# Performance work log

Hardware: AMD Instinct MI355X
Metric: run time of the kernel (lower is better)

Reference implementation:

```python
import jax, jax.numpy as jnp
import numpy as np

B, T, V, E_DIM, M_DIM, H = 32, 256, 10000, 300, 128, 256


def setup_inputs() -> dict:
    key = jax.random.key(0)
    ks = jax.random.split(key, 8)
    sc = 0.05
    words = jax.random.randint(ks[0], (B, T), 0, V)            # int token ids, 0 = pad
    midis = jax.random.normal(ks[1], (B, T, M_DIM), dtype=jnp.float32)
    E  = jax.random.normal(ks[2], (V, E_DIM), dtype=jnp.float32) * sc   # embedding table
    Wm = jax.random.normal(ks[3], (M_DIM, E_DIM), dtype=jnp.float32) * sc  # midi Dense
    bm = jnp.zeros((E_DIM,), jnp.float32)
    Wx = jax.random.normal(ks[4], (E_DIM, 3 * H), dtype=jnp.float32) * sc  # GRU input kernel [z|r|h]
    bx = jnp.zeros((3 * H,), jnp.float32)
    U  = jax.random.normal(ks[5], (H, 3 * H), dtype=jnp.float32) * sc      # GRU recurrent kernel
    bu = jnp.zeros((3 * H,), jnp.float32)                                  # recurrent bias (reset_after)
    Wo = jax.random.normal(ks[6], (H, V), dtype=jnp.float32) * sc          # output Dense
    bo = jnp.zeros((V,), jnp.float32)
    return {"words": words, "midis": midis, "E": E, "Wm": Wm, "bm": bm,
            "Wx": Wx, "bx": bx, "U": U, "bu": bu, "Wo": Wo, "bo": bo}


def _gru_masked(x, mask, Wx, bx, U, bu):
    """Keras GRU (reset_after=True) with mask carry-through. x: [B,T,E], mask: [B,T] bool."""
    gx = x @ Wx + bx                      # [B,T,3H] precomputed input gates
    gx_t = jnp.swapaxes(gx, 0, 1)         # [T,B,3H]
    m_t = mask.T                          # [T,B]
    h0 = jnp.zeros((x.shape[0], H), x.dtype)

    def step(h, inp):
        g, m = inp
        gh = h @ U + bu                   # [B,3H]
        xz, xr, xn = jnp.split(g, 3, axis=-1)
        hz, hr, hn = jnp.split(gh, 3, axis=-1)
        z = jax.nn.sigmoid(xz + hz)
        r = jax.nn.sigmoid(xr + hr)
        n = jnp.tanh(xn + r * hn)         # reset_after: r applied to recurrent projection
        h_new = z * h + (1.0 - z) * n
        h_new = jnp.where(m[:, None], h_new, h)  # masked step: carry state/output
        return h_new, h_new

    h_last, seq = jax.lax.scan(step, h0, (gx_t, m_t))
    return jnp.swapaxes(seq, 0, 1), h_last  # [B,T,H], [B,H]


def reference(words, midis, E, Wm, bm, Wx, bx, U, bu, Wo, bo):
    mask = words != 0                      # Embedding(mask_zero=True).compute_mask
    x = E[words] + (midis @ Wm + bm)       # [B,T,E] fused embedding + dense add
    seq, _ = _gru_masked(x, mask, Wx, bx, U, bu)
    return seq @ Wo + bo                   # [B,T,V] logits
```

## Files before the change

kernel.cpp:

```cpp
#include <hip/hip_runtime.h>
#include <hip/hip_fp16.h>

typedef unsigned short ushort_t;
typedef short bf16x8 __attribute__((ext_vector_type(8)));
typedef float f32x4 __attribute__((ext_vector_type(4)));
typedef _Float16 f16x8 __attribute__((ext_vector_type(8)));

#define B_SZ 32
#define T_SZ 256
#define V_SZ 10000
#define E_DIM 300
#define M_DIM 128
#define H_SZ 256

__device__ __forceinline__ ushort_t f2bf(float f) {
  unsigned u = __float_as_uint(f);
  unsigned r = u + 0x7fffu + ((u >> 16) & 1u);
  return (ushort_t)(r >> 16);
}

__device__ __forceinline__ void stage16(const void* g, void* l) {
  __builtin_amdgcn_global_load_lds((const __attribute__((address_space(1))) void*)g,
                                   (__attribute__((address_space(3))) void*)l, 16, 0, 0);
}

__global__ void k_cast_bf16(const float* __restrict__ in, ushort_t* __restrict__ out, int n) {
  int i = blockIdx.x * blockDim.x + threadIdx.x;
  if (i < n) out[i] = f2bf(in[i]);
}

template <int MODE>
__global__ void k_transpose_cast(const float* __restrict__ in, ushort_t* __restrict__ out,
                                 int R, int C, int Rp, int Cp) {
  __shared__ float tile[32][33];
  int c0 = blockIdx.x * 32, r0 = blockIdx.y * 32;
  int tx = threadIdx.x, ty = threadIdx.y;
#pragma unroll
  for (int i = 0; i < 32; i += 8) {
    int r = r0 + ty + i, c = c0 + tx;
    tile[ty + i][tx] = (r < R && c < C) ? in[(size_t)r * C + c] : 0.f;
  }
  __syncthreads();
#pragma unroll
  for (int i = 0; i < 32; i += 8) {
    int c = c0 + ty + i, r = r0 + tx;
    if (c < Cp && r < Rp) {
      float v = tile[tx][ty + i];
      if (MODE == 0) {
        out[(size_t)c * Rp + r] = f2bf(v);
      } else {
        __half h = __float2half(v);
        out[(size_t)c * Rp + r] = *(ushort_t*)&h;
      }
    }
  }
}

__global__ void k_xfuse(const float* __restrict__ xtmp, const float* __restrict__ E,
                        const int* __restrict__ words, ushort_t* __restrict__ xb) {
  int m = blockIdx.x;
  int kp = threadIdx.x;
  int w = words[m];
  float v = 0.f;
  if (kp < E_DIM) v = xtmp[(size_t)m * 320 + kp] + E[(size_t)w * E_DIM + kp];
  xb[(size_t)m * 320 + kp] = f2bf(v);
}

__global__ __launch_bounds__(256, 2) void k_gemm_bt(
    const ushort_t* __restrict__ A, const ushort_t* __restrict__ BT,
    const float* __restrict__ bias, float* __restrict__ C,
    int M, int K, int Nreal, int ldc) {
  __shared__ __align__(16) ushort_t As[128 * 64];
  __shared__ __align__(16) ushort_t Bs[128 * 64];
  const int tid = threadIdx.x;
  const int lane = tid & 63;
  const int w = tid >> 6;
  const int wr = w >> 1, wc = w & 1;
  const int m0 = blockIdx.x * 128;
  const int n0 = blockIdx.y * 128;

  f32x4 acc[4][4];
#pragma unroll
  for (int i = 0; i < 4; ++i)
#pragma unroll
    for (int j = 0; j < 4; ++j) acc[i][j] = (f32x4){0.f, 0.f, 0.f, 0.f};

  const int chunk_l = w * 64 + lane;

  for (int k0 = 0; k0 < K; k0 += 64) {
    __syncthreads();
#pragma unroll
    for (int it = 0; it < 4; ++it) {
      const int chunk = it * 256 + chunk_l;
      const int row = chunk >> 3, c = chunk & 7;
      const int base = it * 256 + w * 64;
      stage16(A + (size_t)(m0 + row) * K + k0 + c * 8, (void*)(As + base * 8));
      stage16(BT + (size_t)(n0 + row) * K + k0 + c * 8, (void*)(Bs + base * 8));
    }
    __syncthreads();

    bf16x8 af[4][2], bfr[4][2];
#pragma unroll
    for (int mi = 0; mi < 4; ++mi) {
      int r = wr * 64 + mi * 16 + (lane & 15);
#pragma unroll
      for (int kk = 0; kk < 2; ++kk) {
        int c16 = kk * 4 + (lane >> 4);
        af[mi][kk] = *(const bf16x8*)(As + r * 64 + c16 * 8);
      }
    }
#pragma unroll
    for (int ni = 0; ni < 4; ++ni) {
      int r = wc * 64 + ni * 16 + (lane & 15);
#pragma unroll
      for (int kk = 0; kk < 2; ++kk) {
        int c16 = kk * 4 + (lane >> 4);
        bfr[ni][kk] = *(const bf16x8*)(Bs + r * 64 + c16 * 8);
      }
    }
#pragma unroll
    for (int mi = 0; mi < 4; ++mi)
#pragma unroll
      for (int ni = 0; ni < 4; ++ni)
#pragma unroll
        for (int kk = 0; kk < 2; ++kk)
          acc[mi][ni] = __builtin_amdgcn_mfma_f32_16x16x32_bf16(af[mi][kk], bfr[ni][kk],
                                                                acc[mi][ni], 0, 0, 0);
  }

  const int rbase = m0 + wr * 64 + (lane >> 4) * 4;
  const int cbase = n0 + wc * 64 + (lane & 15);
#pragma unroll
  for (int ni = 0; ni < 4; ++ni) {
    int n = cbase + ni * 16;
    if (n < Nreal) {
      float bn = bias[n];
#pragma unroll
      for (int mi = 0; mi < 4; ++mi) {
#pragma unroll
        for (int rg = 0; rg < 4; ++rg) {
          int mrow = rbase + mi * 16 + rg;
          C[(size_t)mrow * ldc + n] = acc[mi][ni][rg] + bn;
        }
      }
    }
  }
}

__global__ __launch_bounds__(512, 2) void k_gru(
    const float* __restrict__ gx, const ushort_t* __restrict__ UT,
    const float* __restrict__ bu, const int* __restrict__ words,
    ushort_t* __restrict__ seqb) {
  const int b = blockIdx.x;
  const int tid = threadIdx.x;
  const int lane = tid & 63;
  const int w = tid >> 6;

  __shared__ __align__(16) _Float16 hlds[16 * 256];
  __shared__ float ghbuf[768];
  __shared__ int words_s[T_SZ];

  for (int i = tid; i < 16 * 256; i += 512) hlds[i] = (_Float16)0.f;
  if (tid < T_SZ) words_s[tid] = words[b * T_SZ + tid];

  f16x8 Ufrag[6][8];
  {
    const int n0 = w * 96;
    const ushort_t* src = UT + (size_t)(n0 + (lane & 15)) * 256 + (lane >> 4) * 8;
#pragma unroll
    for (int ni = 0; ni < 6; ++ni) {
#pragma unroll
      for (int kk = 0; kk < 8; ++kk)
        Ufrag[ni][kk] = *(const f16x8*)(src + (size_t)ni * 16 * 256 + kk * 32);
    }
  }
  float buz = 0.f, bur = 0.f, bun = 0.f;
  if (tid < H_SZ) {
    buz = bu[tid];
    bur = bu[H_SZ + tid];
    bun = bu[2 * H_SZ + tid];
  }
  __syncthreads();

  const float* gxp = gx + (size_t)b * T_SZ * 768;
  float gxz = 0.f, gxr = 0.f, gxn = 0.f;
  if (tid < H_SZ) {
    gxz = gxp[tid];
    gxr = gxp[H_SZ + tid];
    gxn = gxp[2 * H_SZ + tid];
  }
  float h_old = 0.f;

  const int arow = lane & 15;
  const int abase = arow * 512;
  const int asub = lane >> 4;
  const int aswz = arow & 7;

  for (int t = 0; t < T_SZ; ++t) {
    float gxz_n = 0.f, gxr_n = 0.f, gxn_n = 0.f;
    if (t + 1 < T_SZ && tid < H_SZ) {
      const float* g1 = gxp + (size_t)(t + 1) * 768;
      gxz_n = g1[tid];
      gxr_n = g1[H_SZ + tid];
      gxn_n = g1[2 * H_SZ + tid];
    }

    f32x4 acc[6];
#pragma unroll
    for (int ni = 0; ni < 6; ++ni) acc[ni] = (f32x4){0.f, 0.f, 0.f, 0.f};
#pragma unroll
    for (int kk = 0; kk < 8; ++kk) {
      int c = kk * 4 + asub;
      f16x8 afrag = *(const f16x8*)((const char*)hlds + abase + ((c ^ aswz) << 4));
#pragma unroll
      for (int ni = 0; ni < 6; ++ni)
        acc[ni] = __builtin_amdgcn_mfma_f32_16x16x32_f16(afrag, Ufrag[ni][kk], acc[ni], 0, 0, 0);
    }
    if (lane < 16) {
      const int nb = w * 96 + lane;
#pragma unroll
      for (int ni = 0; ni < 6; ++ni) ghbuf[nb + ni * 16] = acc[ni][0];
    }
    __syncthreads();

    if (tid < H_SZ) {
      float hz = ghbuf[tid] + buz;
      float hr = ghbuf[H_SZ + tid] + bur;
      float hn = ghbuf[2 * H_SZ + tid] + bun;
      float z = 1.f / (1.f + __expf(-(gxz + hz)));
      float r = 1.f / (1.f + __expf(-(gxr + hr)));
      float nv = 2.f / (1.f + __expf(-2.f * (gxn + r * hn))) - 1.f;
      float hnew = (words_s[t] != 0) ? (z * h_old + (1.f - z) * nv) : h_old;
      h_old = hnew;
      seqb[((size_t)b * T_SZ + t) * H_SZ + tid] = f2bf(hnew);
      hlds[tid] = (_Float16)hnew;
    }
    __syncthreads();
    gxz = gxz_n;
    gxr = gxr_n;
    gxn = gxn_n;
  }
}

extern "C" void kernel_launch(void* const* d_in, const int* in_sizes, int n_in,
                              void* d_out, int out_size, void* d_ws, size_t ws_size,
                              hipStream_t stream) {
  const int*   words = (const int*)d_in[0];
  const float* midis = (const float*)d_in[1];
  const float* E     = (const float*)d_in[2];
  const float* Wm    = (const float*)d_in[3];
  const float* bm    = (const float*)d_in[4];
  const float* Wx    = (const float*)d_in[5];
  const float* bx    = (const float*)d_in[6];
  const float* U     = (const float*)d_in[7];
  const float* bu    = (const float*)d_in[8];
  const float* Wo    = (const float*)d_in[9];
  const float* bo    = (const float*)d_in[10];
  float* out = (float*)d_out;

  const int MT = B_SZ * T_SZ;
  size_t off = 0;
  auto alloc = [&](size_t bytes) -> void* {
    void* p = (char*)d_ws + off;
    off += (bytes + 255) & ~(size_t)255;
    return p;
  };
  ushort_t* mid_b = (ushort_t*)alloc((size_t)MT * 128 * 2);
  ushort_t* WmT   = (ushort_t*)alloc((size_t)384 * 128 * 2);
  float*    xtmp  = (float*)   alloc((size_t)MT * 320 * 4);
  ushort_t* x_b   = (ushort_t*)alloc((size_t)MT * 320 * 2);
  ushort_t* WxT   = (ushort_t*)alloc((size_t)768 * 320 * 2);
  float*    gx    = (float*)   alloc((size_t)MT * 768 * 4);
  ushort_t* UT    = (ushort_t*)alloc((size_t)768 * 256 * 2);
  ushort_t* seq_b = (ushort_t*)alloc((size_t)MT * 256 * 2);
  ushort_t* WoT   = (ushort_t*)alloc((size_t)10112 * 256 * 2);
  (void)ws_size;

  k_cast_bf16<<<(MT * 128 + 255) / 256, 256, 0, stream>>>(midis, mid_b, MT * 128);
  k_transpose_cast<0><<<dim3(12, 4),  dim3(32, 8), 0, stream>>>(Wm, WmT, 128, 300, 128, 384);
  k_transpose_cast<0><<<dim3(24, 10), dim3(32, 8), 0, stream>>>(Wx, WxT, 300, 768, 320, 768);
  k_transpose_cast<0><<<dim3(316, 8), dim3(32, 8), 0, stream>>>(Wo, WoT, 256, 10000, 256, 10112);
  k_transpose_cast<1><<<dim3(24, 8),  dim3(32, 8), 0, stream>>>(U, UT, 256, 768, 256, 768);

  k_gemm_bt<<<dim3(64, 3), 256, 0, stream>>>(mid_b, WmT, bm, xtmp, MT, 128, 300, 320);
  k_xfuse<<<MT, 320, 0, stream>>>(xtmp, E, words, x_b);
  k_gemm_bt<<<dim3(64, 6), 256, 0, stream>>>(x_b, WxT, bx, gx, MT, 320, 768, 768);
  k_gru<<<B_SZ, 512, 0, stream>>>(gx, UT, bu, words, seq_b);
  k_gemm_bt<<<dim3(64, 79), 256, 0, stream>>>(seq_b, WoT, bo, out, MT, 256, 10000, 10000);
}
```

Baseline: 471.2 us.

## Remap GRU gate columns per wave and double-buffer hidden state to drop barrier

Each wave now owns matching z/r/n columns for 32 hidden units, so it can do the gate nonlinearities directly from its MFMA accumulators instead of going through a shared gh buffer. The hidden state is double-buffered in LDS, which leaves one __syncthreads per timestep instead of two. The recurrent bias is folded into the accumulator initialisation. In exchange, only 16 lanes per wave do the elementwise work, each handling two units, and gx is loaded with a strided pattern.

```diff
diff --git a/kernel.cpp b/kernel.cpp
--- a/kernel.cpp
+++ b/kernel.cpp
@@ -156,89 +156,94 @@
   const int lane = tid & 63;
   const int w = tid >> 6;
 
-  __shared__ __align__(16) _Float16 hlds[16 * 256];
-  __shared__ float ghbuf[768];
+  __shared__ __align__(16) _Float16 hbuf[2][16 * 256];
   __shared__ int words_s[T_SZ];
 
-  for (int i = tid; i < 16 * 256; i += 512) hlds[i] = (_Float16)0.f;
+  for (int i = tid; i < 2 * 16 * 256; i += 512) hbuf[0][i] = (_Float16)0.f;
   if (tid < T_SZ) words_s[tid] = words[b * T_SZ + tid];
 
+  const int jb = w * 32;
+  int colbase[6] = {jb, jb + 16, H_SZ + jb, H_SZ + jb + 16, 2 * H_SZ + jb, 2 * H_SZ + jb + 16};
+
   f16x8 Ufrag[6][8];
-  {
-    const int n0 = w * 96;
-    const ushort_t* src = UT + (size_t)(n0 + (lane & 15)) * 256 + (lane >> 4) * 8;
-#pragma unroll
-    for (int ni = 0; ni < 6; ++ni) {
-#pragma unroll
-      for (int kk = 0; kk < 8; ++kk)
-        Ufrag[ni][kk] = *(const f16x8*)(src + (size_t)ni * 16 * 256 + kk * 32);
-    }
-  }
-  float buz = 0.f, bur = 0.f, bun = 0.f;
-  if (tid < H_SZ) {
-    buz = bu[tid];
-    bur = bu[H_SZ + tid];
-    bun = bu[2 * H_SZ + tid];
-  }
-  __syncthreads();
-
+#pragma unroll
+  for (int ni = 0; ni < 6; ++ni) {
+    const ushort_t* src = UT + (size_t)(colbase[ni] + (lane & 15)) * 256 + (lane >> 4) * 8;
+#pragma unroll
+    for (int kk = 0; kk < 8; ++kk)
+      Ufrag[ni][kk] = *(const f16x8*)(src + kk * 32);
+  }
+  float bub[6];
+#pragma unroll
+  for (int ni = 0; ni < 6; ++ni) bub[ni] = (lane < 16) ? bu[colbase[ni] + lane] : 0.f;
+
+  const int j0 = jb + (lane & 15);
+  const int j1 = j0 + 16;
   const float* gxp = gx + (size_t)b * T_SZ * 768;
-  float gxz = 0.f, gxr = 0.f, gxn = 0.f;
-  if (tid < H_SZ) {
-    gxz = gxp[tid];
-    gxr = gxp[H_SZ + tid];
-    gxn = gxp[2 * H_SZ + tid];
-  }
-  float h_old = 0.f;
+
+  float gz0 = 0.f, gz1 = 0.f, gr0 = 0.f, gr1 = 0.f, gn0 = 0.f, gn1 = 0.f;
+  if (lane < 16) {
+    gz0 = gxp[j0];          gz1 = gxp[j1];
+    gr0 = gxp[H_SZ + j0];   gr1 = gxp[H_SZ + j1];
+    gn0 = gxp[2 * H_SZ + j0]; gn1 = gxp[2 * H_SZ + j1];
+  }
+  float h0 = 0.f, h1 = 0.f;
 
   const int arow = lane & 15;
   const int abase = arow * 512;
   const int asub = lane >> 4;
   const int aswz = arow & 7;
 
+  int p = 0;
+  __syncthreads();
+
   for (int t = 0; t < T_SZ; ++t) {
-    float gxz_n = 0.f, gxr_n = 0.f, gxn_n = 0.f;
-    if (t + 1 < T_SZ && tid < H_SZ) {
+    float gz0n = 0.f, gz1n = 0.f, gr0n = 0.f, gr1n = 0.f, gn0n = 0.f, gn1n = 0.f;
+    if (t + 1 < T_SZ && lane < 16) {
       const float* g1 = gxp + (size_t)(t + 1) * 768;
-      gxz_n = g1[tid];
-      gxr_n = g1[H_SZ + tid];
-      gxn_n = g1[2 * H_SZ + tid];
+      gz0n = g1[j0];          gz1n = g1[j1];
+      gr0n = g1[H_SZ + j0];   gr1n = g1[H_SZ + j1];
+      gn0n = g1[2 * H_SZ + j0]; gn1n = g1[2 * H_SZ + j1];
     }
 
     f32x4 acc[6];
 #pragma unroll
-    for (int ni = 0; ni < 6; ++ni) acc[ni] = (f32x4){0.f, 0.f, 0.f, 0.f};
+    for (int ni = 0; ni < 6; ++ni) acc[ni] = (f32x4){bub[ni], 0.f, 0.f, 0.f};
+    const _Float16* hp = hbuf[p];
 #pragma unroll
     for (int kk = 0; kk < 8; ++kk) {
       int c = kk * 4 + asub;
-      f16x8 afrag = *(const f16x8*)((const char*)hlds + abase + ((c ^ aswz) << 4));
+      f16x8 afrag = *(const f16x8*)((const char*)hp + abase + ((c ^ aswz) << 4));
 #pragma unroll
       for (int ni = 0; ni < 6; ++ni)
         acc[ni] = __builtin_amdgcn_mfma_f32_16x16x32_f16(afrag, Ufrag[ni][kk], acc[ni], 0, 0, 0);
     }
+
     if (lane < 16) {
-      const int nb = w * 96 + lane;
-#pragma unroll
-      for (int ni = 0; ni < 6; ++ni) ghbuf[nb + ni * 16] = acc[ni][0];
+      const int wv = words_s[t];
+      float z0 = 1.f / (1.f + __expf(-(gz0 + acc[0][0])));
+      float z1 = 1.f / (1.f + __expf(-(gz1 + acc[1][0])));
+      float r0 = 1.f / (1.f + __expf(-(gr0 + acc[2][0])));
+      float r1 = 1.f / (1.f + __expf(-(gr1 + acc[3][0])));
+      float n0 = 2.f / (1.f + __expf(-2.f * (gn0 + r0 * acc[4][0]))) - 1.f;
+      float n1 = 2.f / (1.f + __expf(-2.f * (gn1 + r1 * acc[5][0]))) - 1.f;
+      float hn0 = (wv != 0) ? (z0 * h0 + (1.f - z0) * n0) : h0;
+      float hn1 = (wv != 0) ? (z1 * h1 + (1.f - z1) * n1) : h1;
+      h0 = hn0;
+      h1 = hn1;
+      const size_t row = (size_t)b * T_SZ + t;
+      seqb[row * H_SZ + j0] = f2bf(hn0);
+      seqb[row * H_SZ + j1] = f2bf(hn1);
+      _Float16* hq = hbuf[p ^ 1];
+      hq[j0] = (_Float16)hn0;
+      hq[j1] = (_Float16)hn1;
     }
     __syncthreads();
-
-    if (tid < H_SZ) {
-      float hz = ghbuf[tid] + buz;
-      float hr = ghbuf[H_SZ + tid] + bur;
-      float hn = ghbuf[2 * H_SZ + tid] + bun;
-      float z = 1.f / (1.f + __expf(-(gxz + hz)));
-      float r = 1.f / (1.f + __expf(-(gxr + hr)));
-      float nv = 2.f / (1.f + __expf(-2.f * (gxn + r * hn))) - 1.f;
-      float hnew = (words_s[t] != 0) ? (z * h_old + (1.f - z) * nv) : h_old;
-      h_old = hnew;
-      seqb[((size_t)b * T_SZ + t) * H_SZ + tid] = f2bf(hnew);
-      hlds[tid] = (_Float16)hnew;
-    }
-    __syncthreads();
-    gxz = gxz_n;
-    gxr = gxr_n;
-    gxn = gxn_n;
+    p ^= 1;
+
+    gz0 = gz0n; gz1 = gz1n;
+    gr0 = gr0n; gr1 = gr1n;
+    gn0 = gn0n; gn1 = gn1n;
   }
 }
 
```

Measured after the change: 828.3 us. +75.8%, slower.
